# Optimization experiments

Hardware: AMD Instinct MI355X
Metric: run time of the kernel (lower is better)

The kernel has to match this reference:

```python
import jax, jax.numpy as jnp
import numpy as np

V = 50288; D = 768; L = 12; SPLIT = 6; L_LORA = L - SPLIT
NSTATE = 64; HDIM = 64
DIN = 2 * D                         # expand=2 -> 1536
H = DIN // HDIM                     # 24 heads
K = 4                               # depthwise conv kernel
DPROJ = 2 * DIN + 2 * NSTATE + H    # 3224
CONVD = DIN + 2 * NSTATE            # 1664
R = 8; LORA_SCALE = 2.0             # alpha/rank = 2r/r
EPS = 1e-5


def _rms(x, w):
    return x * jax.lax.rsqrt(jnp.mean(x * x, axis=-1, keepdims=True) + EPS) * w


def _ssm_scan(dt, A, Bm, Cm, xh):
    # dt:[B,T,H]  A:[H]  Bm,Cm:[B,T,N]  xh:[B,T,H,P]
    dA = jnp.exp(dt * A)
    def step(h, inp):
        dA_t, dt_t, B_t, C_t, x_t = inp
        h = dA_t[:, :, None, None] * h + (dt_t[..., None] * x_t)[..., None] * B_t[:, None, None, :]
        return h, jnp.einsum('bhpn,bn->bhp', h, C_t)
    h0 = jnp.zeros((dt.shape[0], H, HDIM, NSTATE), dt.dtype)
    xs = tuple(jnp.moveaxis(a, 1, 0) for a in (dA, dt, Bm, Cm, xh))
    _, ys = jax.lax.scan(step, h0, xs)
    return jnp.moveaxis(ys, 0, 1)  # [B,T,H,P]


@jax.checkpoint
def _mixer(u, in_w, cw, cb, dtb, A_log, Dsk, gw, out_w):
    # Mamba2 selective-scan block (ngroups=1, no biases on projections)
    Bsz, T, _ = u.shape
    zxbcdt = u @ in_w.T                              # [B,T,DPROJ]
    z = zxbcdt[..., :DIN]
    xBC = zxbcdt[..., DIN:DIN + CONVD]
    dt = zxbcdt[..., DIN + CONVD:]
    xp = jnp.pad(xBC, ((0, 0), (K - 1, 0), (0, 0)))  # causal depthwise conv1d
    xBC = jax.nn.silu(cb + sum(cw[:, k] * xp[:, k:k + T] for k in range(K)))
    xh = xBC[..., :DIN].reshape(Bsz, T, H, HDIM)
    Bm = xBC[..., DIN:DIN + NSTATE]
    Cm = xBC[..., DIN + NSTATE:]
    dt = jax.nn.softplus(dt + dtb)
    y = _ssm_scan(dt, -jnp.exp(A_log), Bm, Cm, xh) + Dsk[None, None, :, None] * xh
    y = _rms(y.reshape(Bsz, T, DIN) * jax.nn.silu(z), gw)   # gated RMSNorm
    return y @ out_w.T


def _run_base(x, res, p):
    def step(carry, q):
        x, res = carry
        res = x + res
        h = _mixer(_rms(res, q['nw']), q['iw'], q['cw'], q['cb'], q['dtb'],
                   q['al'], q['dk'], q['gw'], q['ow'])
        return (h, res), None
    (x, res), _ = jax.lax.scan(step, (x, res), p)
    return x, res


def _run_lora(x, res, p):
    def step(carry, q):
        x, res = carry
        res = x + res
        iw = q['iw'] + LORA_SCALE * (q['ibw'] @ q['iaw'])   # LoRALinear effective weight
        ow = q['ow'] + LORA_SCALE * (q['obw'] @ q['oaw'])
        h = _mixer(_rms(res, q['nw']), iw, q['cw'], q['cb'], q['dtb'],
                   q['al'], q['dk'], q['gw'], ow)
        return (h, res), None
    (x, res), _ = jax.lax.scan(step, (x, res), p)
    return x, res


def _rope(x, loop_i):
    # LoopRoPE: rotate interleaved pairs of hidden dims by angle theta_i * loop_i
    inv_freq = 1.0 / (10000.0 ** (jnp.arange(0, D, 2, dtype=jnp.float32) / D))
    f = loop_i * inv_freq
    cos_v = jnp.repeat(jnp.cos(f), 2)
    sin_v = jnp.repeat(jnp.sin(f), 2)
    x1, x2 = x[..., ::2], x[..., 1::2]
    rot = jnp.stack([-x2, x1], axis=-1).reshape(x.shape)
    return x * cos_v + rot * sin_v


def _forward(input_ids, n_loops, embedding, norm_w, in_w, conv_w, conv_b, dt_bias, A_log,
             D_skip, gnorm_w, out_w, lora_in_A, lora_in_B, lora_out_A, lora_out_B,
             core_in_w, core_conv_w, core_conv_b, core_dt_bias, core_A_log, core_D,
             core_gnorm_w, core_out_w, loop_norm_w, lifeline_gate, norm_f_w, lm_head_w):
    base = {'nw': norm_w[:SPLIT], 'iw': in_w[:SPLIT], 'cw': conv_w[:SPLIT], 'cb': conv_b[:SPLIT],
            'dtb': dt_bias[:SPLIT], 'al': A_log[:SPLIT], 'dk': D_skip[:SPLIT],
            'gw': gnorm_w[:SPLIT], 'ow': out_w[:SPLIT]}
    lora = {'nw': norm_w[SPLIT:], 'iw': in_w[SPLIT:], 'cw': conv_w[SPLIT:], 'cb': conv_b[SPLIT:],
            'dtb': dt_bias[SPLIT:], 'al': A_log[SPLIT:], 'dk': D_skip[SPLIT:],
            'gw': gnorm_w[SPLIT:], 'ow': out_w[SPLIT:],
            'iaw': lora_in_A, 'ibw': lora_in_B, 'oaw': lora_out_A, 'obw': lora_out_B}
    x = embedding[input_ids]                       # [B,T,D]
    res = jnp.zeros_like(x)                        # residual=None -> zeros
    x, res = _run_base(x, res, base)               # frozen layers [0:6]
    x, res = _run_lora(x, res, lora)               # LoRA layers [6:12]
    x_prompt = jax.lax.stop_gradient(x)            # x.clone().detach()
    for i in range(int(n_loops)):
        x = x + lifeline_gate * x_prompt           # lifeline injection
        x = _rope(x, float(i))                     # loop-index RoPE
        x, res = _run_lora(x, res, lora)           # run_lora recursion body
        x = x + _mixer(x, core_in_w, core_conv_w, core_conv_b, core_dt_bias,
                       core_A_log, core_D, core_gnorm_w, core_out_w)  # mamba2_core
        x = _rms(x, loop_norm_w)                   # loop_norm
    h = _rms(x + res, norm_f_w)                    # norm_f(x, residual, prenorm=False)
    return h @ lm_head_w.T                         # lm_head logits [B,T,V]


def setup_inputs() -> dict:
    key = jax.random.key(0)
    ks = iter(jax.random.split(key, 64))
    f32 = jnp.float32
    def w(shape, s=0.02):
        return (s * jax.random.normal(next(ks), shape)).astype(f32)
    inp = {
        'input_ids': jax.random.randint(next(ks), (2, 512), 0, 50277, dtype=jnp.int32),
        'n_loops': 3,
        'embedding': w((V, D)),
        'norm_w': jnp.ones((L, D), f32),
        'in_w': w((L, DPROJ, D)),
        'conv_w': w((L, CONVD, K), 0.2),
        'conv_b': jnp.zeros((L, CONVD), f32),
        'dt_bias': w((L, H), 0.5),
        'A_log': jnp.log(1.0 + 15.0 * jax.random.uniform(next(ks), (L, H))).astype(f32),
        'D_skip': jnp.ones((L, H), f32),
        'gnorm_w': jnp.ones((L, DIN), f32),
        'out_w': w((L, D, DIN)),
        'lora_in_A': w((L_LORA, R, D), 0.05),
        'lora_in_B': w((L_LORA, DPROJ, R), 0.05),
        'lora_out_A': w((L_LORA, R, DIN), 0.05),
        'lora_out_B': w((L_LORA, D, R), 0.05),
        'core_in_w': w((DPROJ, D)),
        'core_conv_w': w((CONVD, K), 0.2),
        'core_conv_b': jnp.zeros((CONVD,), f32),
        'core_dt_bias': w((H,), 0.5),
        'core_A_log': jnp.log(1.0 + 15.0 * jax.random.uniform(next(ks), (H,))).astype(f32),
        'core_D': jnp.ones((H,), f32),
        'core_gnorm_w': jnp.ones((DIN,), f32),
        'core_out_w': w((D, DIN)),
        'loop_norm_w': jnp.ones((D,), f32),
        'lifeline_gate': jnp.ones((D,), f32),
        'norm_f_w': jnp.ones((D,), f32),
        'lm_head_w': w((V, D)),
    }
    return inp


def reference(input_ids, n_loops, embedding, norm_w, in_w, conv_w, conv_b, dt_bias, A_log,
              D_skip, gnorm_w, out_w, lora_in_A, lora_in_B, lora_out_A, lora_out_B,
              core_in_w, core_conv_w, core_conv_b, core_dt_bias, core_A_log, core_D,
              core_gnorm_w, core_out_w, loop_norm_w, lifeline_gate, norm_f_w, lm_head_w):
    return _forward(input_ids, n_loops, embedding, norm_w, in_w, conv_w, conv_b, dt_bias,
                    A_log, D_skip, gnorm_w, out_w, lora_in_A, lora_in_B, lora_out_A,
                    lora_out_B, core_in_w, core_conv_w, core_conv_b, core_dt_bias,
                    core_A_log, core_D, core_gnorm_w, core_out_w, loop_norm_w,
                    lifeline_gate, norm_f_w, lm_head_w)
```

## Files before the change

kernel.cpp:

```cpp
#include <hip/hip_runtime.h>
#include <math.h>

constexpr int Bsz   = 2;
constexpr int Tseq  = 512;
constexpr int Mtok  = Bsz * Tseq;
constexpr int Dm    = 768;
constexpr int DINc  = 1536;
constexpr int Hn    = 24;
constexpr int NS    = 64;
constexpr int KC    = 4;
constexpr int DPROJc = 2*DINc + 2*NS + Hn;
constexpr int CONVDc = DINc + 2*NS;
constexpr int NL    = 12;
constexpr int SPL   = 6;
constexpr int LLO   = 6;
constexpr int NCH   = 8;
constexpr int Vv    = 50288;
constexpr float EPSc = 1e-5f;
constexpr int NLOOPS = 3;

#define DEVI __device__ __forceinline__

typedef _Float16 f16x8 __attribute__((ext_vector_type(8)));
typedef float    f32x4 __attribute__((ext_vector_type(4)));

DEVI float siluf(float x){ return x / (1.0f + expf(-x)); }
DEVI float softplusf(float x){ return (x > 20.0f) ? x : log1pf(expf(x)); }
DEVI unsigned short f2h(float f){
  union { _Float16 h; unsigned short u; } c;
  c.h = (_Float16)f;
  return c.u;
}
DEVI float h2f(unsigned short u){
  union { unsigned short u; _Float16 h; } c;
  c.u = u; return (float)c.h;
}

DEVI void gload16(const void* g, void* l){
  __builtin_amdgcn_global_load_lds(
      (const __attribute__((address_space(1))) void*)g,
      (__attribute__((address_space(3))) void*)l, 16, 0, 0);
}

DEVI float blk_reduce256(float v, float* sh){
  #pragma unroll
  for (int o = 32; o; o >>= 1) v += __shfl_down(v, o);
  int lane = threadIdx.x & 63, w = threadIdx.x >> 6;
  if (lane == 0) sh[w] = v;
  __syncthreads();
  return sh[0] + sh[1] + sh[2] + sh[3];
}

__global__ void k_embed(const int* __restrict__ ids, const float* __restrict__ emb,
                        float* __restrict__ x){
  int m = blockIdx.x;
  int id = ids[m];
  const float4* src = (const float4*)(emb + (size_t)id * Dm);
  float4* dst = (float4*)(x + (size_t)m * Dm);
  int i = threadIdx.x;
  dst[i] = src[i];
}

__global__ void k_f2h(const float* __restrict__ in, unsigned short* __restrict__ out, int n4){
  int e = blockIdx.x*256 + threadIdx.x;
  if (e >= n4) return;
  float4 v = ((const float4*)in)[e];
  ushort4 o; o.x=f2h(v.x); o.y=f2h(v.y); o.z=f2h(v.z); o.w=f2h(v.w);
  ((ushort4*)out)[e] = o;
}

__global__ __launch_bounds__(256) void k_addrms(const float* __restrict__ xin,
    float* __restrict__ res, unsigned short* __restrict__ ub,
    const float* __restrict__ w){
  int m = blockIdx.x, tid = threadIdx.x;
  __shared__ float sh[4];
  const float* xr = xin + (size_t)m*Dm;
  float* rr = res + (size_t)m*Dm;
  float r[3]; float ss = 0.f;
  #pragma unroll
  for (int k=0;k<3;k++){ int e = tid + k*256; float v = xr[e] + rr[e]; r[k]=v; ss += v*v; }
  ss = blk_reduce256(ss, sh);
  float rs = 1.0f / sqrtf(ss/(float)Dm + EPSc);
  #pragma unroll
  for (int k=0;k<3;k++){
    int e = tid + k*256;
    rr[e] = r[k];
    ub[(size_t)m*Dm+e] = f2h(r[k]*rs*w[e]);
  }
}

__global__ __launch_bounds__(256) void k_addrms_p(const float* __restrict__ part,
    float* __restrict__ res, unsigned short* __restrict__ ub,
    const float* __restrict__ w){
  int m = blockIdx.x, tid = threadIdx.x;
  __shared__ float sh[4];
  const size_t tot = (size_t)Mtok*Dm;
  float* rr = res + (size_t)m*Dm;
  float r[3]; float ss = 0.f;
  #pragma unroll
  for (int k=0;k<3;k++){
    int e = tid + k*256;
    size_t idx = (size_t)m*Dm + e;
    float v = rr[e] + part[idx] + part[tot+idx] + part[2*tot+idx] + part[3*tot+idx];
    r[k]=v; ss += v*v;
  }
  ss = blk_reduce256(ss, sh);
  float rs = 1.0f / sqrtf(ss/(float)Dm + EPSc);
  #pragma unroll
  for (int k=0;k<3;k++){
    int e = tid + k*256;
    rr[e] = r[k];
    ub[(size_t)m*Dm+e] = f2h(r[k]*rs*w[e]);
  }
}

__global__ void k_sum_xp(const float* __restrict__ part, float* __restrict__ x,
                         float* __restrict__ xp){
  size_t e = (size_t)blockIdx.x*256 + threadIdx.x;
  const size_t tot = (size_t)Mtok*Dm;
  if (e >= tot) return;
  float v = part[e] + part[tot+e] + part[2*tot+e] + part[3*tot+e];
  x[e] = v; xp[e] = v;
}

__global__ void k_f2h_sum(const float* __restrict__ part, float* __restrict__ x,
                          unsigned short* __restrict__ ub){
  size_t e = (size_t)blockIdx.x*256 + threadIdx.x;
  const size_t tot = (size_t)Mtok*Dm;
  if (e >= tot) return;
  float v = part[e] + part[tot+e] + part[2*tot+e] + part[3*tot+e];
  x[e] = v; ub[e] = f2h(v);
}

__global__ __launch_bounds__(256) void k_rms_p(const float* __restrict__ part,
    float* __restrict__ x, const float* __restrict__ w){
  int m = blockIdx.x, tid = threadIdx.x;
  __shared__ float sh[4];
  const size_t tot = (size_t)Mtok*Dm;
  float* xr = x + (size_t)m*Dm;
  float r[3]; float ss = 0.f;
  #pragma unroll
  for (int k=0;k<3;k++){
    int e = tid + k*256;
    size_t idx = (size_t)m*Dm + e;
    float v = xr[e] + part[idx] + part[tot+idx] + part[2*tot+idx] + part[3*tot+idx];
    r[k]=v; ss += v*v;
  }
  ss = blk_reduce256(ss, sh);
  float rs = 1.0f / sqrtf(ss/(float)Dm + EPSc);
  #pragma unroll
  for (int k=0;k<3;k++){ int e = tid + k*256; xr[e] = r[k]*rs*w[e]; }
}

__global__ __launch_bounds__(128) void k_liferope(float* __restrict__ x,
    const float* __restrict__ xp, const float* __restrict__ gate, float iF){
  int m = blockIdx.x, tid = threadIdx.x;
  float* xr = x + (size_t)m*Dm;
  const float* pr = xp + (size_t)m*Dm;
  #pragma unroll
  for (int k=0;k<3;k++){
    int j = tid + k*128;
    int d0 = 2*j, d1 = d0+1;
    float v0 = xr[d0] + gate[d0]*pr[d0];
    float v1 = xr[d1] + gate[d1]*pr[d1];
    float invf = expf(-9.210340371976184f * ((float)(2*j) * (1.0f/768.0f)));
    float f = iF * invf;
    float cv = cosf(f), sv = sinf(f);
    xr[d0] = v0*cv - v1*sv;
    xr[d1] = v1*cv + v0*sv;
  }
}

__global__ __launch_bounds__(256) void k_gemm_h(
    const unsigned short* __restrict__ A,
    const unsigned short* __restrict__ Bw,
    void* __restrict__ Cv, int Nd, int Kd, int outmode){
  alignas(16) __shared__ unsigned short lA[2][128*64];
  alignas(16) __shared__ unsigned short lB[2][128*64];
  const int tid  = threadIdx.x;
  const int lane = tid & 63;
  const int wv   = tid >> 6;
  const int wm   = wv >> 1, wn = wv & 1;
  const int gx = gridDim.x, gy = gridDim.y;
  const int nwg = gx*gy;
  const int flat = blockIdx.x + gx*blockIdx.y;
  const int q = nwg >> 3, r = nwg & 7;
  const int xcd = flat & 7, pos = flat >> 3;
  const int lg = (xcd < r ? xcd*(q+1) : r*(q+1) + (xcd - r)*q) + pos;
  const int m_idx = lg % gy, n_idx = lg / gy;
  const int n0 = n_idx * 128;
  const int m0 = m_idx * 128;
  const int KS = gridDim.z;
  const int kchunk = Kd / KS;
  const int kbeg = blockIdx.z * kchunk;
  const int nsteps = kchunk / 64;

  f32x4 acc[4][4] = {};

  auto stage = [&](int buf, int k0){
    #pragma unroll
    for (int i=0;i<4;i++){
      int seg = tid + i*256;
      int row = seg >> 3;
      int c8  = (seg & 7) ^ (row & 7);
      gload16(A + (size_t)(m0 + row)*Kd + k0 + c8*8, &lA[buf][seg*8]);
      int rn = n0 + row; rn = (rn < Nd) ? rn : (Nd - 1);
      gload16(Bw + (size_t)rn*Kd + k0 + c8*8, &lB[buf][seg*8]);
    }
  };

  stage(0, kbeg);
  for (int t=0; t<nsteps; ++t){
    const int cur = t & 1;
    if (t+1 < nsteps){
      stage(cur^1, kbeg + (t+1)*64);
      __builtin_amdgcn_sched_barrier(0);
      asm volatile("s_waitcnt vmcnt(8)" ::: "memory");
    } else {
      asm volatile("s_waitcnt vmcnt(0)" ::: "memory");
    }
    __builtin_amdgcn_s_barrier();
    __builtin_amdgcn_sched_barrier(0);
    #pragma unroll
    for (int kk=0; kk<2; kk++){
      f16x8 af[4], bfr[4];
      #pragma unroll
      for (int f=0; f<4; f++){
        int rowa = wm*64 + f*16 + (lane & 15);
        int ba = rowa*128 + ((kk*64 + (lane>>4)*16) ^ ((rowa & 7) << 4));
        af[f] = *(const f16x8*)((const char*)&lA[cur][0] + ba);
        int rowb = wn*64 + f*16 + (lane & 15);
        int bb = rowb*128 + ((kk*64 + (lane>>4)*16) ^ ((rowb & 7) << 4));
        bfr[f] = *(const f16x8*)((const char*)&lB[cur][0] + bb);
      }
      #pragma unroll
      for (int fm=0; fm<4; fm++)
        #pragma unroll
        for (int fn=0; fn<4; fn++)
          acc[fm][fn] = __builtin_amdgcn_mfma_f32_16x16x32_f16(af[fm], bfr[fn], acc[fm][fn], 0, 0, 0);
    }
    __builtin_amdgcn_s_barrier();
  }

  #pragma unroll
  for (int fm=0; fm<4; fm++){
    int mbase = m0 + wm*64 + fm*16 + ((lane>>4)<<2);
    #pragma unroll
    for (int fn=0; fn<4; fn++){
      int n = n0 + wn*64 + fn*16 + (lane & 15);
      if (n < Nd){
        #pragma unroll
        for (int rr=0;rr<4;rr++){
          size_t idx = (size_t)(mbase + rr)*Nd + n;
          float v = acc[fm][fn][rr];
          if (outmode == 0){
            float* Cb = (float*)Cv + (size_t)blockIdx.z*((size_t)Mtok*Nd);
            Cb[idx] = v;
          } else if (outmode == 1){
            ((float*)Cv)[idx] = v;
          } else {
            ((unsigned short*)Cv)[idx] = f2h(v);
          }
        }
      }
    }
  }
}

__global__ void k_prep_in(const float* __restrict__ W12, const float* __restrict__ Wc,
    const float* __restrict__ lA, const float* __restrict__ lB,
    unsigned short* __restrict__ out){
  const int tot4 = DPROJc*Dm/4;
  int e4 = blockIdx.x*256 + threadIdx.x;
  if (e4 >= tot4) return;
  int l = blockIdx.y;
  const float* W = (l < 12) ? W12 + (size_t)l*DPROJc*Dm : Wc;
  const int k4n = Dm/4;
  int n = e4 / k4n, k4 = e4 - n*k4n;
  float4 wv = *(const float4*)(W + (size_t)n*Dm + k4*4);
  float s0=wv.x, s1=wv.y, s2=wv.z, s3=wv.w;
  if (l >= SPL && l < 12){
    int ll = l - SPL;
    const float* Bl = lB + (size_t)ll*DPROJc*8;
    const float* Al = lA + (size_t)ll*8*Dm;
    #pragma unroll
    for (int r=0;r<8;r++){
      float b = 2.0f * Bl[n*8+r];
      float4 a = *(const float4*)(Al + (size_t)r*Dm + k4*4);
      s0 += b*a.x; s1 += b*a.y; s2 += b*a.z; s3 += b*a.w;
    }
  }
  ushort4 o; o.x=f2h(s0); o.y=f2h(s1); o.z=f2h(s2); o.w=f2h(s3);
  ((ushort4*)(out + (size_t)l*DPROJc*Dm))[e4] = o;
}

__global__ void k_prep_out(const float* __restrict__ W12, const float* __restrict__ Wc,
    const float* __restrict__ lA, const float* __restrict__ lB,
    unsigned short* __restrict__ out){
  const int tot4 = Dm*DINc/4;
  int e4 = blockIdx.x*256 + threadIdx.x;
  if (e4 >= tot4) return;
  int l = blockIdx.y;
  const float* W = (l < 12) ? W12 + (size_t)l*Dm*DINc : Wc;
  const int k4n = DINc/4;
  int n = e4 / k4n, k4 = e4 - n*k4n;
  float4 wv = *(const float4*)(W + (size_t)n*DINc + k4*4);
  float s0=wv.x, s1=wv.y, s2=wv.z, s3=wv.w;
  if (l >= SPL && l < 12){
    int ll = l - SPL;
    const float* Bl = lB + (size_t)ll*Dm*8;
    const float* Al = lA + (size_t)ll*8*DINc;
    #pragma unroll
    for (int r=0;r<8;r++){
      float b = 2.0f * Bl[n*8+r];
      float4 a = *(const float4*)(Al + (size_t)r*DINc + k4*4);
      s0 += b*a.x; s1 += b*a.y; s2 += b*a.z; s3 += b*a.w;
    }
  }
  ushort4 o; o.x=f2h(s0); o.y=f2h(s1); o.z=f2h(s2); o.w=f2h(s3);
  ((ushort4*)(out + (size_t)l*Dm*DINc))[e4] = o;
}

DEVI f16x8 ldfrag(const unsigned short (*T)[72], int row, int k0){
  return *(const f16x8*)&T[row][k0];
}

__global__ __launch_bounds__(256) void k_s1(const unsigned short* __restrict__ zxh,
    const float* __restrict__ cw, const float* __restrict__ cb,
    const float* __restrict__ dtb, const float* __restrict__ alog,
    float* __restrict__ S, float* __restrict__ ctot){
  int bh = blockIdx.x; int b = bh / Hn, h = bh % Hn; int c = blockIdx.y;
  __shared__ unsigned short XT[64][72];
  __shared__ unsigned short BwT[64][72];
  __shared__ float wv[64];
  int tid = threadIdx.x;
  int base_m = b*Tseq + c*64;
  if (tid < 64){
    float Av = -expf(alog[h]);
    float zdt = h2f(zxh[(size_t)(base_m+tid)*DPROJc + DINc + CONVDc + h]) + dtb[h];
    float dt = softplusf(zdt);
    float s = dt * Av;
    #pragma unroll
    for (int o=1;o<64;o<<=1){ float v = __shfl_up(s, o); if (tid >= o) s += v; }
    if (tid == 63) ctot[bh*NCH + c] = s;
    float ce = __shfl(s, 63);
    wv[tid] = expf(ce - s) * dt;
  }
  __syncthreads();
  int ch = tid & 63;
  int t0 = (tid >> 6) * 16;
  int tl = c*64 + t0;
  {
    int cc = h*64 + ch;
    float4 w4 = *(const float4*)&cw[cc*KC];
    float bias = cb[cc];
    const unsigned short* zp = zxh + (size_t)base_m*DPROJc + DINc + cc;
    float v0 = (tl >= 3) ? h2f(zp[(long)(t0-3)*DPROJc]) : 0.f;
    float v1 = (tl >= 2) ? h2f(zp[(long)(t0-2)*DPROJc]) : 0.f;
    float v2 = (tl >= 1) ? h2f(zp[(long)(t0-1)*DPROJc]) : 0.f;
    #pragma unroll
    for (int i=0;i<16;i++){
      float v3 = h2f(zp[(long)(t0+i)*DPROJc]);
      float o = bias + w4.x*v0 + w4.y*v1 + w4.z*v2 + w4.w*v3;
      XT[ch][t0+i] = f2h(siluf(o));
      v0=v1; v1=v2; v2=v3;
    }
  }
  {
    int cc = DINc + ch;
    float4 w4 = *(const float4*)&cw[cc*KC];
    float bias = cb[cc];
    const unsigned short* zp = zxh + (size_t)base_m*DPROJc + DINc + cc;
    float v0 = (tl >= 3) ? h2f(zp[(long)(t0-3)*DPROJc]) : 0.f;
    float v1 = (tl >= 2) ? h2f(zp[(long)(t0-2)*DPROJc]) : 0.f;
    float v2 = (tl >= 1) ? h2f(zp[(long)(t0-1)*DPROJc]) : 0.f;
    #pragma unroll
    for (int i=0;i<16;i++){
      float v3 = h2f(zp[(long)(t0+i)*DPROJc]);
      float o = bias + w4.x*v0 + w4.y*v1 + w4.z*v2 + w4.w*v3;
      BwT[ch][t0+i] = f2h(siluf(o) * wv[t0+i]);
      v0=v1; v1=v2; v2=v3;
    }
  }
  __syncthreads();
  int lane = tid & 63, wid = tid >> 6, wmp = wid >> 1, wnn = wid & 1;
  f32x4 acc[2][2] = {};
  #pragma unroll
  for (int kk=0; kk<2; kk++){
    int k0 = kk*32 + (lane>>4)*8;
    f16x8 a[2], bf[2];
    #pragma unroll
    for (int f=0; f<2; f++){
      a[f]  = ldfrag(XT,  wmp*32 + f*16 + (lane&15), k0);
      bf[f] = ldfrag(BwT, wnn*32 + f*16 + (lane&15), k0);
    }
    #pragma unroll
    for (int fm=0; fm<2; fm++)
      #pragma unroll
      for (int fn=0; fn<2; fn++)
        acc[fm][fn] = __builtin_amdgcn_mfma_f32_16x16x32_f16(a[fm], bf[fn], acc[fm][fn], 0, 0, 0);
  }
  float* Sb = S + ((size_t)(bh*NCH + c))*4096;
  #pragma unroll
  for (int fm=0; fm<2; fm++)
    #pragma unroll
    for (int fn=0; fn<2; fn++)
      #pragma unroll
      for (int rg=0; rg<4; rg++){
        int p = wmp*32 + fm*16 + ((lane>>4)<<2) + rg;
        int n = wnn*32 + fn*16 + (lane&15);
        Sb[p*64 + n] = acc[fm][fn][rg];
      }
}

__global__ void k_s2(const float* __restrict__ S, const float* __restrict__ ctot,
                     float* __restrict__ hst){
  int gid = blockIdx.x*256 + threadIdx.x;
  int bh = gid >> 12; int e = gid & 4095;
  float hv = 0.f;
  #pragma unroll
  for (int c=0;c<NCH;c++){
    size_t idx = ((size_t)(bh*NCH + c))*4096 + e;
    hst[idx] = hv;
    float Ac = expf(ctot[bh*NCH + c]);
    hv = Ac*hv + S[idx];
  }
}

__global__ __launch_bounds__(256) void k_s3(const unsigned short* __restrict__ zxh,
    const float* __restrict__ cw, const float* __restrict__ cb,
    const float* __restrict__ dtb, const float* __restrict__ alog,
    const float* __restrict__ hst, const float* __restrict__ Dsk,
    unsigned short* __restrict__ y){
  int bh = blockIdx.x; int b = bh / Hn, h = bh % Hn; int c = blockIdx.y;
  __shared__ unsigned short Ch[64][72];
  __shared__ unsigned short Bh[64][72];
  __shared__ unsigned short XhT[64][72];
  __shared__ unsigned short hT[64][72];
  __shared__ unsigned short Mh[64][72];
  __shared__ float cumS[64], dtS[64];
  int tid = threadIdx.x;
  int base_m = b*Tseq + c*64;
  if (tid < 64){
    float Av = -expf(alog[h]);
    float zdt = h2f(zxh[(size_t)(base_m+tid)*DPROJc + DINc + CONVDc + h]) + dtb[h];
    float dt = softplusf(zdt);
    float s = dt * Av;
    #pragma unroll
    for (int o=1;o<64;o<<=1){ float v = __shfl_up(s, o); if (tid >= o) s += v; }
    cumS[tid] = s;
    dtS[tid]  = dt;
  }
  int ch = tid & 63;
  int t0 = (tid >> 6) * 16;
  int tl = c*64 + t0;
  {
    int cc = h*64 + ch;
    float4 w4 = *(const float4*)&cw[cc*KC];
    float bias = cb[cc];
    const unsigned short* zp = zxh + (size_t)base_m*DPROJc + DINc + cc;
    float v0 = (tl >= 3) ? h2f(zp[(long)(t0-3)*DPROJc]) : 0.f;
    float v1 = (tl >= 2) ? h2f(zp[(long)(t0-2)*DPROJc]) : 0.f;
    float v2 = (tl >= 1) ? h2f(zp[(long)(t0-1)*DPROJc]) : 0.f;
    #pragma unroll
    for (int i=0;i<16;i++){
      float v3 = h2f(zp[(long)(t0+i)*DPROJc]);
      float o = bias + w4.x*v0 + w4.y*v1 + w4.z*v2 + w4.w*v3;
      XhT[ch][t0+i] = f2h(siluf(o));
      v0=v1; v1=v2; v2=v3;
    }
  }
  {
    int cc = DINc + ch;
    float4 w4 = *(const float4*)&cw[cc*KC];
    float bias = cb[cc];
    const unsigned short* zp = zxh + (size_t)base_m*DPROJc + DINc + cc;
    float v0 = (tl >= 3) ? h2f(zp[(long)(t0-3)*DPROJc]) : 0.f;
    float v1 = (tl >= 2) ? h2f(zp[(long)(t0-2)*DPROJc]) : 0.f;
    float v2 = (tl >= 1) ? h2f(zp[(long)(t0-1)*DPROJc]) : 0.f;
    #pragma unroll
    for (int i=0;i<16;i++){
      float v3 = h2f(zp[(long)(t0+i)*DPROJc]);
      float o = bias + w4.x*v0 + w4.y*v1 + w4.z*v2 + w4.w*v3;
      Bh[t0+i][ch] = f2h(siluf(o));
      v0=v1; v1=v2; v2=v3;
    }
  }
  {
    int cc = DINc + NS + ch;
    float4 w4 = *(const float4*)&cw[cc*KC];
    float bias = cb[cc];
    const unsigned short* zp = zxh + (size_t)base_m*DPROJc + DINc + cc;
    float v0 = (tl >= 3) ? h2f(zp[(long)(t0-3)*DPROJc]) : 0.f;
    float v1 = (tl >= 2) ? h2f(zp[(long)(t0-2)*DPROJc]) : 0.f;
    float v2 = (tl >= 1) ? h2f(zp[(long)(t0-1)*DPROJc]) : 0.f;
    #pragma unroll
    for (int i=0;i<16;i++){
      float v3 = h2f(zp[(long)(t0+i)*DPROJc]);
      float o = bias + w4.x*v0 + w4.y*v1 + w4.z*v2 + w4.w*v3;
      Ch[t0+i][ch] = f2h(siluf(o));
      v0=v1; v1=v2; v2=v3;
    }
  }
  {
    const float* hb = hst + ((size_t)(bh*NCH + c))*4096;
    for (int e4 = tid; e4 < 1024; e4 += 256){
      float4 hv = ((const float4*)hb)[e4];
      int p = (e4 << 2) >> 6, n = (e4 << 2) & 63;
      ushort4 o; o.x=f2h(hv.x); o.y=f2h(hv.y); o.z=f2h(hv.z); o.w=f2h(hv.w);
      *(ushort4*)&hT[p][n] = o;
    }
  }
  __syncthreads();
  int lane = tid & 63, wid = tid >> 6, wmt = wid >> 1, wns = wid & 1;
  f32x4 g[2][2] = {};
  #pragma unroll
  for (int kk=0; kk<2; kk++){
    int k0 = kk*32 + (lane>>4)*8;
    f16x8 a[2], bf[2];
    #pragma unroll
    for (int f=0; f<2; f++){
      a[f]  = ldfrag(Ch, wmt*32 + f*16 + (lane&15), k0);
      bf[f] = ldfrag(Bh, wns*32 + f*16 + (lane&15), k0);
    }
    #pragma unroll
    for (int fm=0; fm<2; fm++)
      #pragma unroll
      for (int fn=0; fn<2; fn++)
        g[fm][fn] = __builtin_amdgcn_mfma_f32_16x16x32_f16(a[fm], bf[fn], g[fm][fn], 0, 0, 0);
  }
  #pragma unroll
  for (int fm=0; fm<2; fm++)
    #pragma unroll
    for (int fn=0; fn<2; fn++)
      #pragma unroll
      for (int rg=0; rg<4; rg++){
        int t = wmt*32 + fm*16 + ((lane>>4)<<2) + rg;
        int s = wns*32 + fn*16 + (lane&15);
        float val = (s <= t) ? expf(cumS[t] - cumS[s]) * dtS[s] * g[fm][fn][rg] : 0.f;
        Mh[t][s] = f2h(val);
      }
  __syncthreads();
  f32x4 aL[2][2] = {}, aS[2][2] = {};
  #pragma unroll
  for (int kk=0; kk<2; kk++){
    int k0 = kk*32 + (lane>>4)*8;
    f16x8 m_[2], x_[2], c_[2], h_[2];
    #pragma unroll
    for (int f=0; f<2; f++){
      m_[f] = ldfrag(Mh,  wmt*32 + f*16 + (lane&15), k0);
      x_[f] = ldfrag(XhT, wns*32 + f*16 + (lane&15), k0);
      c_[f] = ldfrag(Ch,  wmt*32 + f*16 + (lane&15), k0);
      h_[f] = ldfrag(hT,  wns*32 + f*16 + (lane&15), k0);
    }
    #pragma unroll
    for (int fm=0; fm<2; fm++)
      #pragma unroll
      for (int fn=0; fn<2; fn++){
        aL[fm][fn] = __builtin_amdgcn_mfma_f32_16x16x32_f16(m_[fm], x_[fn], aL[fm][fn], 0, 0, 0);
        aS[fm][fn] = __builtin_amdgcn_mfma_f32_16x16x32_f16(c_[fm], h_[fn], aS[fm][fn], 0, 0, 0);
      }
  }
  float Dh = Dsk[h];
  #pragma unroll
  for (int fm=0; fm<2; fm++)
    #pragma unroll
    for (int fn=0; fn<2; fn++)
      #pragma unroll
      for (int rg=0; rg<4; rg++){
        int t = wmt*32 + fm*16 + ((lane>>4)<<2) + rg;
        int p = wns*32 + fn*16 + (lane&15);
        float Pt = expf(cumS[t]);
        float xv = h2f(XhT[p][t]);
        float o = aL[fm][fn][rg] + Pt*aS[fm][fn][rg] + Dh*xv;
        y[(size_t)(base_m+t)*DINc + h*64 + p] = f2h(o);
      }
}

__global__ __launch_bounds__(256) void k_gate(const unsigned short* __restrict__ zxh,
    const unsigned short* __restrict__ y, unsigned short* __restrict__ yb,
    const float* __restrict__ gw){
  int m = blockIdx.x, tid = threadIdx.x;
  __shared__ float sh[4];
  const unsigned short* zr = zxh + (size_t)m*DPROJc;
  const unsigned short* yr = y + (size_t)m*DINc;
  float g[6]; float ss = 0.f;
  #pragma unroll
  for (int k=0;k<6;k++){
    int e = tid + k*256;
    float z = h2f(zr[e]);
    float v = h2f(yr[e]) * siluf(z);
    g[k] = v; ss += v*v;
  }
  ss = blk_reduce256(ss, sh);
  float rs = 1.0f / sqrtf(ss/(float)DINc + EPSc);
  #pragma unroll
  for (int k=0;k<6;k++){
    int e = tid + k*256;
    yb[(size_t)m*DINc + e] = f2h(g[k]*rs*gw[e]);
  }
}

struct WSP {
  float *x,*res,*xp,*ctot,*Sc,*hst,*part;
  unsigned short *zxh,*yh,*ub,*yb,*wib,*wob,*whb;
};

static void run_mixer_h(hipStream_t st, const WSP& w, const unsigned short* ub_in,
    const unsigned short* iw, const float* cw, const float* cb, const float* dtb,
    const float* al, const float* dk, const float* gw, const unsigned short* ow){
  dim3 gIn((DPROJc + 127)/128, Mtok/128, 1);
  k_gemm_h<<<gIn, 256, 0, st>>>(ub_in, iw, w.zxh, DPROJc, Dm, 2);
  k_s1<<<dim3(Bsz*Hn, NCH), 256, 0, st>>>(w.zxh, cw, cb, dtb, al, w.Sc, w.ctot);
  k_s2<<<(Bsz*Hn*4096)/256, 256, 0, st>>>(w.Sc, w.ctot, w.hst);
  k_s3<<<dim3(Bsz*Hn, NCH), 256, 0, st>>>(w.zxh, cw, cb, dtb, al, w.hst, dk, w.yh);
  k_gate<<<Mtok, 256, 0, st>>>(w.zxh, w.yh, w.yb, gw);
  dim3 gOut(Dm/128, Mtok/128, 4);
  k_gemm_h<<<gOut, 256, 0, st>>>(w.yb, ow, w.part, Dm, DINc, 0);
}

extern "C" void kernel_launch(void* const* d_in, const int* in_sizes, int n_in,
                              void* d_out, int out_size, void* d_ws, size_t ws_size,
                              hipStream_t stream){
  const int*   ids        = (const int*)  d_in[0];
  const float* emb        = (const float*)d_in[2];
  const float* norm_w     = (const float*)d_in[3];
  const float* in_w       = (const float*)d_in[4];
  const float* conv_w     = (const float*)d_in[5];
  const float* conv_b     = (const float*)d_in[6];
  const float* dt_bias    = (const float*)d_in[7];
  const float* A_log      = (const float*)d_in[8];
  const float* D_skip     = (const float*)d_in[9];
  const float* gnorm_w    = (const float*)d_in[10];
  const float* out_w      = (const float*)d_in[11];
  const float* lora_in_A  = (const float*)d_in[12];
  const float* lora_in_B  = (const float*)d_in[13];
  const float* lora_out_A = (const float*)d_in[14];
  const float* lora_out_B = (const float*)d_in[15];
  const float* core_in_w  = (const float*)d_in[16];
  const float* core_conv_w= (const float*)d_in[17];
  const float* core_conv_b= (const float*)d_in[18];
  const float* core_dtb   = (const float*)d_in[19];
  const float* core_A_log = (const float*)d_in[20];
  const float* core_D     = (const float*)d_in[21];
  const float* core_gw    = (const float*)d_in[22];
  const float* core_out_w = (const float*)d_in[23];
  const float* loop_norm_w= (const float*)d_in[24];
  const float* life_gate  = (const float*)d_in[25];
  const float* norm_f_w   = (const float*)d_in[26];
  const float* lm_head_w  = (const float*)d_in[27];
  (void)in_sizes; (void)n_in; (void)out_size; (void)ws_size;

  char* pb = (char*)d_ws;
  auto balloc = [&](size_t bytes){
    char* q = pb; pb += (bytes + 255) & ~(size_t)255; return q;
  };
  WSP w;
  w.x    = (float*)balloc((size_t)Mtok*Dm*4);
  w.res  = (float*)balloc((size_t)Mtok*Dm*4);
  w.xp   = (float*)balloc((size_t)Mtok*Dm*4);
  w.ctot = (float*)balloc((size_t)Bsz*Hn*NCH*4);
  w.Sc   = (float*)balloc((size_t)Bsz*Hn*NCH*4096*4);
  w.hst  = (float*)balloc((size_t)Bsz*Hn*NCH*4096*4);
  w.part = (float*)balloc((size_t)4*Mtok*Dm*4);
  w.zxh  = (unsigned short*)balloc((size_t)Mtok*DPROJc*2);
  w.yh   = (unsigned short*)balloc((size_t)Mtok*DINc*2);
  w.ub   = (unsigned short*)balloc((size_t)Mtok*Dm*2);
  w.yb   = (unsigned short*)balloc((size_t)Mtok*DINc*2);

  const size_t IWN = (size_t)DPROJc*Dm;
  const size_t OWN = (size_t)Dm*DINc;
  const size_t HWN = (size_t)Vv*Dm;
  w.wib = (unsigned short*)balloc(13*IWN*2);
  w.wob = (unsigned short*)balloc(13*OWN*2);
  w.whb = (unsigned short*)balloc(HWN*2);

  k_prep_in<<<dim3((IWN/4 + 255)/256, 13), 256, 0, stream>>>(
      in_w, core_in_w, lora_in_A, lora_in_B, w.wib);
  k_prep_out<<<dim3((OWN/4 + 255)/256, 13), 256, 0, stream>>>(
      out_w, core_out_w, lora_out_A, lora_out_B, w.wob);
  k_f2h<<<(HWN/4 + 255)/256, 256, 0, stream>>>(lm_head_w, w.whb, (int)(HWN/4));

  k_embed<<<Mtok, 192, 0, stream>>>(ids, emb, w.x);
  hipMemsetAsync(w.res, 0, (size_t)Mtok*Dm*sizeof(float), stream);

  const size_t totMD = (size_t)Mtok*Dm;

  auto mixer_l = [&](int l){
    run_mixer_h(stream, w, w.ub,
        w.wib + (size_t)l*IWN, conv_w + (size_t)l*CONVDc*KC, conv_b + (size_t)l*CONVDc,
        dt_bias + (size_t)l*Hn, A_log + (size_t)l*Hn, D_skip + (size_t)l*Hn,
        gnorm_w + (size_t)l*DINc, w.wob + (size_t)l*OWN);
  };
  k_addrms<<<Mtok, 256, 0, stream>>>(w.x, w.res, w.ub, norm_w);
  mixer_l(0);
  for (int l=1; l<NL; l++){
    k_addrms_p<<<Mtok, 256, 0, stream>>>(w.part, w.res, w.ub, norm_w + (size_t)l*Dm);
    mixer_l(l);
  }
  k_sum_xp<<<(totMD + 255)/256, 256, 0, stream>>>(w.part, w.x, w.xp);
  for (int i=0;i<NLOOPS;i++){
    k_liferope<<<Mtok, 128, 0, stream>>>(w.x, w.xp, life_gate, (float)i);
    k_addrms<<<Mtok, 256, 0, stream>>>(w.x, w.res, w.ub, norm_w + (size_t)SPL*Dm);
    mixer_l(SPL);
    for (int l=SPL+1; l<NL; l++){
      k_addrms_p<<<Mtok, 256, 0, stream>>>(w.part, w.res, w.ub, norm_w + (size_t)l*Dm);
      mixer_l(l);
    }
    k_f2h_sum<<<(totMD + 255)/256, 256, 0, stream>>>(w.part, w.x, w.ub);
    run_mixer_h(stream, w, w.ub,
        w.wib + 12*IWN, core_conv_w, core_conv_b, core_dtb, core_A_log, core_D,
        core_gw, w.wob + 12*OWN);
    k_rms_p<<<Mtok, 256, 0, stream>>>(w.part, w.x, loop_norm_w);
  }
  k_addrms<<<Mtok, 256, 0, stream>>>(w.x, w.res, w.ub, norm_f_w);
  dim3 gHead((Vv + 127)/128, Mtok/128, 1);
  k_gemm_h<<<gHead, 256, 0, stream>>>(w.ub, w.whb, d_out, Vv, Dm, 1);
}
```

Before: 2.752 ms.

## Fuse chunked SSD scan stages and gated RMSNorm into one per-head kernel

Replaces the three chunked-scan kernels (k_s1, k_s2, k_s3) and the gate kernel with a single k_ssd kernel per (batch, head). Each block loops over the chunks sequentially and carries the inter-chunk state in shared memory. The gated output's sum of squares is accumulated into a per-row buffer with atomics. The gnorm weight is folded into the output-projection weights at prep time, and the RMS scale is applied in the output GEMM epilogue. This removes several launches per mixer and the round-trips of state and intermediate y through global memory. In exchange, the scan grid shrinks from 384 blocks to 48 blocks that run the chunks serially.

```diff
diff --git a/kernel.cpp b/kernel.cpp
--- a/kernel.cpp
+++ b/kernel.cpp
@@ -71,7 +71,7 @@
 
 __global__ __launch_bounds__(256) void k_addrms(const float* __restrict__ xin,
     float* __restrict__ res, unsigned short* __restrict__ ub,
-    const float* __restrict__ w){
+    const float* __restrict__ w, float* __restrict__ rssum){
   int m = blockIdx.x, tid = threadIdx.x;
   __shared__ float sh[4];
   const float* xr = xin + (size_t)m*Dm;
@@ -80,6 +80,7 @@
   #pragma unroll
   for (int k=0;k<3;k++){ int e = tid + k*256; float v = xr[e] + rr[e]; r[k]=v; ss += v*v; }
   ss = blk_reduce256(ss, sh);
+  if (tid == 0 && rssum) rssum[m] = 0.f;
   float rs = 1.0f / sqrtf(ss/(float)Dm + EPSc);
   #pragma unroll
   for (int k=0;k<3;k++){
@@ -91,7 +92,7 @@
 
 __global__ __launch_bounds__(256) void k_addrms_p(const float* __restrict__ part,
     float* __restrict__ res, unsigned short* __restrict__ ub,
-    const float* __restrict__ w){
+    const float* __restrict__ w, float* __restrict__ rssum){
   int m = blockIdx.x, tid = threadIdx.x;
   __shared__ float sh[4];
   const size_t tot = (size_t)Mtok*Dm;
@@ -105,6 +106,7 @@
     r[k]=v; ss += v*v;
   }
   ss = blk_reduce256(ss, sh);
+  if (tid == 0 && rssum) rssum[m] = 0.f;
   float rs = 1.0f / sqrtf(ss/(float)Dm + EPSc);
   #pragma unroll
   for (int k=0;k<3;k++){
@@ -124,10 +126,11 @@
 }
 
 __global__ void k_f2h_sum(const float* __restrict__ part, float* __restrict__ x,
-                          unsigned short* __restrict__ ub){
+                          unsigned short* __restrict__ ub, float* __restrict__ rssum){
   size_t e = (size_t)blockIdx.x*256 + threadIdx.x;
   const size_t tot = (size_t)Mtok*Dm;
   if (e >= tot) return;
+  if (e < Mtok) rssum[e] = 0.f;
   float v = part[e] + part[tot+e] + part[2*tot+e] + part[3*tot+e];
   x[e] = v; ub[e] = f2h(v);
 }
@@ -174,9 +177,11 @@
 __global__ __launch_bounds__(256) void k_gemm_h(
     const unsigned short* __restrict__ A,
     const unsigned short* __restrict__ Bw,
-    void* __restrict__ Cv, int Nd, int Kd, int outmode){
+    void* __restrict__ Cv, int Nd, int Kd, int outmode,
+    const float* __restrict__ rsrow){
   alignas(16) __shared__ unsigned short lA[2][128*64];
   alignas(16) __shared__ unsigned short lB[2][128*64];
+  __shared__ float lRs[128];
   const int tid  = threadIdx.x;
   const int lane = tid & 63;
   const int wv   = tid >> 6;
@@ -195,6 +200,8 @@
   const int kbeg = blockIdx.z * kchunk;
   const int nsteps = kchunk / 64;
 
+  if (rsrow && tid < 128) lRs[tid] = rsrow[m0 + tid];
+
   f32x4 acc[4][4] = {};
 
   auto stage = [&](int buf, int k0){
@@ -244,7 +251,8 @@
 
   #pragma unroll
   for (int fm=0; fm<4; fm++){
-    int mbase = m0 + wm*64 + fm*16 + ((lane>>4)<<2);
+    int mloc = wm*64 + fm*16 + ((lane>>4)<<2);
+    int mbase = m0 + mloc;
     #pragma unroll
     for (int fn=0; fn<4; fn++){
       int n = n0 + wn*64 + fn*16 + (lane & 15);
@@ -253,6 +261,8 @@
         for (int rr=0;rr<4;rr++){
           size_t idx = (size_t)(mbase + rr)*Nd + n;
           float v = acc[fm][fn][rr];
+          if (rsrow)
+            v *= 1.0f / sqrtf(lRs[mloc + rr]*(1.0f/(float)DINc) + EPSc);
           if (outmode == 0){
             float* Cb = (float*)Cv + (size_t)blockIdx.z*((size_t)Mtok*Nd);
             Cb[idx] = v;
@@ -296,12 +306,14 @@
 
 __global__ void k_prep_out(const float* __restrict__ W12, const float* __restrict__ Wc,
     const float* __restrict__ lA, const float* __restrict__ lB,
+    const float* __restrict__ gnw, const float* __restrict__ core_gw,
     unsigned short* __restrict__ out){
   const int tot4 = Dm*DINc/4;
   int e4 = blockIdx.x*256 + threadIdx.x;
   if (e4 >= tot4) return;
   int l = blockIdx.y;
   const float* W = (l < 12) ? W12 + (size_t)l*Dm*DINc : Wc;
+  const float* gw = (l < 12) ? gnw + (size_t)l*DINc : core_gw;
   const int k4n = DINc/4;
   int n = e4 / k4n, k4 = e4 - n*k4n;
   float4 wv = *(const float4*)(W + (size_t)n*DINc + k4*4);
@@ -317,6 +329,8 @@
       s0 += b*a.x; s1 += b*a.y; s2 += b*a.z; s3 += b*a.w;
     }
   }
+  float4 g4 = *(const float4*)(gw + k4*4);
+  s0 *= g4.x; s1 *= g4.y; s2 *= g4.z; s3 *= g4.w;
   ushort4 o; o.x=f2h(s0); o.y=f2h(s1); o.z=f2h(s2); o.w=f2h(s3);
   ((ushort4*)(out + (size_t)l*Dm*DINc))[e4] = o;
 }
@@ -325,298 +339,203 @@
   return *(const f16x8*)&T[row][k0];
 }
 
-__global__ __launch_bounds__(256) void k_s1(const unsigned short* __restrict__ zxh,
+__global__ __launch_bounds__(256) void k_ssd(const unsigned short* __restrict__ zxh,
     const float* __restrict__ cw, const float* __restrict__ cb,
     const float* __restrict__ dtb, const float* __restrict__ alog,
-    float* __restrict__ S, float* __restrict__ ctot){
-  int bh = blockIdx.x; int b = bh / Hn, h = bh % Hn; int c = blockIdx.y;
-  __shared__ unsigned short XT[64][72];
+    const float* __restrict__ Dsk, unsigned short* __restrict__ g_out,
+    float* __restrict__ rssum){
+  int bh = blockIdx.x; int b = bh / Hn, h = bh % Hn;
+  __shared__ unsigned short XhT[64][72];
+  __shared__ unsigned short Bh [64][72];
   __shared__ unsigned short BwT[64][72];
-  __shared__ float wv[64];
+  __shared__ unsigned short Ch [64][72];
+  __shared__ unsigned short Mh [64][72];
+  __shared__ unsigned short hT [64][72];
+  __shared__ float hS[64][64];
+  __shared__ float cumS[64], dtS[64], wvS[64];
+  __shared__ float AcS;
   int tid = threadIdx.x;
-  int base_m = b*Tseq + c*64;
-  if (tid < 64){
-    float Av = -expf(alog[h]);
-    float zdt = h2f(zxh[(size_t)(base_m+tid)*DPROJc + DINc + CONVDc + h]) + dtb[h];
-    float dt = softplusf(zdt);
-    float s = dt * Av;
-    #pragma unroll
-    for (int o=1;o<64;o<<=1){ float v = __shfl_up(s, o); if (tid >= o) s += v; }
-    if (tid == 63) ctot[bh*NCH + c] = s;
-    float ce = __shfl(s, 63);
-    wv[tid] = expf(ce - s) * dt;
-  }
-  __syncthreads();
+  int lane = tid & 63, wid = tid >> 6, wmt = wid >> 1, wns = wid & 1;
+  for (int e = tid; e < 4096; e += 256) ((float*)hS)[e] = 0.f;
+  float Av = -expf(alog[h]);
+  float Dh = Dsk[h];
   int ch = tid & 63;
   int t0 = (tid >> 6) * 16;
-  int tl = c*64 + t0;
-  {
-    int cc = h*64 + ch;
-    float4 w4 = *(const float4*)&cw[cc*KC];
-    float bias = cb[cc];
-    const unsigned short* zp = zxh + (size_t)base_m*DPROJc + DINc + cc;
-    float v0 = (tl >= 3) ? h2f(zp[(long)(t0-3)*DPROJc]) : 0.f;
-    float v1 = (tl >= 2) ? h2f(zp[(long)(t0-2)*DPROJc]) : 0.f;
-    float v2 = (tl >= 1) ? h2f(zp[(long)(t0-1)*DPROJc]) : 0.f;
-    #pragma unroll
-    for (int i=0;i<16;i++){
-      float v3 = h2f(zp[(long)(t0+i)*DPROJc]);
-      float o = bias + w4.x*v0 + w4.y*v1 + w4.z*v2 + w4.w*v3;
-      XT[ch][t0+i] = f2h(siluf(o));
-      v0=v1; v1=v2; v2=v3;
-    }
-  }
-  {
-    int cc = DINc + ch;
-    float4 w4 = *(const float4*)&cw[cc*KC];
-    float bias = cb[cc];
-    const unsigned short* zp = zxh + (size_t)base_m*DPROJc + DINc + cc;
-    float v0 = (tl >= 3) ? h2f(zp[(long)(t0-3)*DPROJc]) : 0.f;
-    float v1 = (tl >= 2) ? h2f(zp[(long)(t0-2)*DPROJc]) : 0.f;
-    float v2 = (tl >= 1) ? h2f(zp[(long)(t0-1)*DPROJc]) : 0.f;
-    #pragma unroll
-    for (int i=0;i<16;i++){
-      float v3 = h2f(zp[(long)(t0+i)*DPROJc]);
-      float o = bias + w4.x*v0 + w4.y*v1 + w4.z*v2 + w4.w*v3;
-      BwT[ch][t0+i] = f2h(siluf(o) * wv[t0+i]);
-      v0=v1; v1=v2; v2=v3;
-    }
-  }
-  __syncthreads();
-  int lane = tid & 63, wid = tid >> 6, wmp = wid >> 1, wnn = wid & 1;
-  f32x4 acc[2][2] = {};
-  #pragma unroll
-  for (int kk=0; kk<2; kk++){
-    int k0 = kk*32 + (lane>>4)*8;
-    f16x8 a[2], bf[2];
-    #pragma unroll
-    for (int f=0; f<2; f++){
-      a[f]  = ldfrag(XT,  wmp*32 + f*16 + (lane&15), k0);
-      bf[f] = ldfrag(BwT, wnn*32 + f*16 + (lane&15), k0);
+
+  for (int c = 0; c < NCH; ++c){
+    __syncthreads();
+    int base_m = b*Tseq + c*64;
+    int tl = c*64 + t0;
+    if (tid < 64){
+      float zdt = h2f(zxh[(size_t)(base_m+tid)*DPROJc + DINc + CONVDc + h]) + dtb[h];
+      float dt = softplusf(zdt);
+      float s = dt * Av;
+      #pragma unroll
+      for (int o=1;o<64;o<<=1){ float v = __shfl_up(s, o); if (tid >= o) s += v; }
+      cumS[tid] = s; dtS[tid] = dt;
+      float ce = __shfl(s, 63);
+      wvS[tid] = expf(ce - s) * dt;
+      if (tid == 0) AcS = expf(ce);
+    }
+    {
+      int cc = h*64 + ch;
+      float4 w4 = *(const float4*)&cw[cc*KC];
+      float bias = cb[cc];
+      const unsigned short* zp = zxh + (size_t)base_m*DPROJc + DINc + cc;
+      float v0 = (tl >= 3) ? h2f(zp[(long)(t0-3)*DPROJc]) : 0.f;
+      float v1 = (tl >= 2) ? h2f(zp[(long)(t0-2)*DPROJc]) : 0.f;
+      float v2 = (tl >= 1) ? h2f(zp[(long)(t0-1)*DPROJc]) : 0.f;
+      #pragma unroll
+      for (int i=0;i<16;i++){
+        float v3 = h2f(zp[(long)(t0+i)*DPROJc]);
+        float o = bias + w4.x*v0 + w4.y*v1 + w4.z*v2 + w4.w*v3;
+        XhT[ch][t0+i] = f2h(siluf(o));
+        v0=v1; v1=v2; v2=v3;
+      }
+    }
+    {
+      int cc = DINc + ch;
+      float4 w4 = *(const float4*)&cw[cc*KC];
+      float bias = cb[cc];
+      const unsigned short* zp = zxh + (size_t)base_m*DPROJc + DINc + cc;
+      float v0 = (tl >= 3) ? h2f(zp[(long)(t0-3)*DPROJc]) : 0.f;
+      float v1 = (tl >= 2) ? h2f(zp[(long)(t0-2)*DPROJc]) : 0.f;
+      float v2 = (tl >= 1) ? h2f(zp[(long)(t0-1)*DPROJc]) : 0.f;
+      #pragma unroll
+      for (int i=0;i<16;i++){
+        float v3 = h2f(zp[(long)(t0+i)*DPROJc]);
+        float o = bias + w4.x*v0 + w4.y*v1 + w4.z*v2 + w4.w*v3;
+        Bh[t0+i][ch] = f2h(siluf(o));
+        v0=v1; v1=v2; v2=v3;
+      }
+    }
+    {
+      int cc = DINc + NS + ch;
+      float4 w4 = *(const float4*)&cw[cc*KC];
+      float bias = cb[cc];
+      const unsigned short* zp = zxh + (size_t)base_m*DPROJc + DINc + cc;
+      float v0 = (tl >= 3) ? h2f(zp[(long)(t0-3)*DPROJc]) : 0.f;
+      float v1 = (tl >= 2) ? h2f(zp[(long)(t0-2)*DPROJc]) : 0.f;
+      float v2 = (tl >= 1) ? h2f(zp[(long)(t0-1)*DPROJc]) : 0.f;
+      #pragma unroll
+      for (int i=0;i<16;i++){
+        float v3 = h2f(zp[(long)(t0+i)*DPROJc]);
+        float o = bias + w4.x*v0 + w4.y*v1 + w4.z*v2 + w4.w*v3;
+        Ch[t0+i][ch] = f2h(siluf(o));
+        v0=v1; v1=v2; v2=v3;
+      }
+    }
+    for (int e4 = tid; e4 < 1024; e4 += 256){
+      const float* hp = (const float*)hS + e4*4;
+      int p = (e4 << 2) >> 6, n = (e4 << 2) & 63;
+      ushort4 o; o.x=f2h(hp[0]); o.y=f2h(hp[1]); o.z=f2h(hp[2]); o.w=f2h(hp[3]);
+      *(ushort4*)&hT[p][n] = o;
+    }
+    __syncthreads();
+    for (int e = tid; e < 4096; e += 256){
+      int t = e >> 6, n = e & 63;
+      BwT[n][t] = f2h(h2f(Bh[t][n]) * wvS[t]);
+    }
+    f32x4 g[2][2] = {};
+    #pragma unroll
+    for (int kk=0; kk<2; kk++){
+      int k0 = kk*32 + (lane>>4)*8;
+      f16x8 a[2], bf[2];
+      #pragma unroll
+      for (int f=0; f<2; f++){
+        a[f]  = ldfrag(Ch, wmt*32 + f*16 + (lane&15), k0);
+        bf[f] = ldfrag(Bh, wns*32 + f*16 + (lane&15), k0);
+      }
+      #pragma unroll
+      for (int fm=0; fm<2; fm++)
+        #pragma unroll
+        for (int fn=0; fn<2; fn++)
+          g[fm][fn] = __builtin_amdgcn_mfma_f32_16x16x32_f16(a[fm], bf[fn], g[fm][fn], 0, 0, 0);
     }
     #pragma unroll
     for (int fm=0; fm<2; fm++)
       #pragma unroll
       for (int fn=0; fn<2; fn++)
-        acc[fm][fn] = __builtin_amdgcn_mfma_f32_16x16x32_f16(a[fm], bf[fn], acc[fm][fn], 0, 0, 0);
-  }
-  float* Sb = S + ((size_t)(bh*NCH + c))*4096;
-  #pragma unroll
-  for (int fm=0; fm<2; fm++)
-    #pragma unroll
-    for (int fn=0; fn<2; fn++)
-      #pragma unroll
-      for (int rg=0; rg<4; rg++){
-        int p = wmp*32 + fm*16 + ((lane>>4)<<2) + rg;
-        int n = wnn*32 + fn*16 + (lane&15);
-        Sb[p*64 + n] = acc[fm][fn][rg];
-      }
-}
-
-__global__ void k_s2(const float* __restrict__ S, const float* __restrict__ ctot,
-                     float* __restrict__ hst){
-  int gid = blockIdx.x*256 + threadIdx.x;
-  int bh = gid >> 12; int e = gid & 4095;
-  float hv = 0.f;
-  #pragma unroll
-  for (int c=0;c<NCH;c++){
-    size_t idx = ((size_t)(bh*NCH + c))*4096 + e;
-    hst[idx] = hv;
-    float Ac = expf(ctot[bh*NCH + c]);
-    hv = Ac*hv + S[idx];
-  }
-}
-
-__global__ __launch_bounds__(256) void k_s3(const unsigned short* __restrict__ zxh,
-    const float* __restrict__ cw, const float* __restrict__ cb,
-    const float* __restrict__ dtb, const float* __restrict__ alog,
-    const float* __restrict__ hst, const float* __restrict__ Dsk,
-    unsigned short* __restrict__ y){
-  int bh = blockIdx.x; int b = bh / Hn, h = bh % Hn; int c = blockIdx.y;
-  __shared__ unsigned short Ch[64][72];
-  __shared__ unsigned short Bh[64][72];
-  __shared__ unsigned short XhT[64][72];
-  __shared__ unsigned short hT[64][72];
-  __shared__ unsigned short Mh[64][72];
-  __shared__ float cumS[64], dtS[64];
-  int tid = threadIdx.x;
-  int base_m = b*Tseq + c*64;
-  if (tid < 64){
-    float Av = -expf(alog[h]);
-    float zdt = h2f(zxh[(size_t)(base_m+tid)*DPROJc + DINc + CONVDc + h]) + dtb[h];
-    float dt = softplusf(zdt);
-    float s = dt * Av;
-    #pragma unroll
-    for (int o=1;o<64;o<<=1){ float v = __shfl_up(s, o); if (tid >= o) s += v; }
-    cumS[tid] = s;
-    dtS[tid]  = dt;
-  }
-  int ch = tid & 63;
-  int t0 = (tid >> 6) * 16;
-  int tl = c*64 + t0;
-  {
-    int cc = h*64 + ch;
-    float4 w4 = *(const float4*)&cw[cc*KC];
-    float bias = cb[cc];
-    const unsigned short* zp = zxh + (size_t)base_m*DPROJc + DINc + cc;
-    float v0 = (tl >= 3) ? h2f(zp[(long)(t0-3)*DPROJc]) : 0.f;
-    float v1 = (tl >= 2) ? h2f(zp[(long)(t0-2)*DPROJc]) : 0.f;
-    float v2 = (tl >= 1) ? h2f(zp[(long)(t0-1)*DPROJc]) : 0.f;
-    #pragma unroll
-    for (int i=0;i<16;i++){
-      float v3 = h2f(zp[(long)(t0+i)*DPROJc]);
-      float o = bias + w4.x*v0 + w4.y*v1 + w4.z*v2 + w4.w*v3;
-      XhT[ch][t0+i] = f2h(siluf(o));
-      v0=v1; v1=v2; v2=v3;
-    }
-  }
-  {
-    int cc = DINc + ch;
-    float4 w4 = *(const float4*)&cw[cc*KC];
-    float bias = cb[cc];
-    const unsigned short* zp = zxh + (size_t)base_m*DPROJc + DINc + cc;
-    float v0 = (tl >= 3) ? h2f(zp[(long)(t0-3)*DPROJc]) : 0.f;
-    float v1 = (tl >= 2) ? h2f(zp[(long)(t0-2)*DPROJc]) : 0.f;
-    float v2 = (tl >= 1) ? h2f(zp[(long)(t0-1)*DPROJc]) : 0.f;
-    #pragma unroll
-    for (int i=0;i<16;i++){
-      float v3 = h2f(zp[(long)(t0+i)*DPROJc]);
-      float o = bias + w4.x*v0 + w4.y*v1 + w4.z*v2 + w4.w*v3;
-      Bh[t0+i][ch] = f2h(siluf(o));
-      v0=v1; v1=v2; v2=v3;
-    }
-  }
-  {
-    int cc = DINc + NS + ch;
-    float4 w4 = *(const float4*)&cw[cc*KC];
-    float bias = cb[cc];
-    const unsigned short* zp = zxh + (size_t)base_m*DPROJc + DINc + cc;
-    float v0 = (tl >= 3) ? h2f(zp[(long)(t0-3)*DPROJc]) : 0.f;
-    float v1 = (tl >= 2) ? h2f(zp[(long)(t0-2)*DPROJc]) : 0.f;
-    float v2 = (tl >= 1) ? h2f(zp[(long)(t0-1)*DPROJc]) : 0.f;
-    #pragma unroll
-    for (int i=0;i<16;i++){
-      float v3 = h2f(zp[(long)(t0+i)*DPROJc]);
-      float o = bias + w4.x*v0 + w4.y*v1 + w4.z*v2 + w4.w*v3;
-      Ch[t0+i][ch] = f2h(siluf(o));
-      v0=v1; v1=v2; v2=v3;
-    }
-  }
-  {
-    const float* hb = hst + ((size_t)(bh*NCH + c))*4096;
-    for (int e4 = tid; e4 < 1024; e4 += 256){
-      float4 hv = ((const float4*)hb)[e4];
-      int p = (e4 << 2) >> 6, n = (e4 << 2) & 63;
-      ushort4 o; o.x=f2h(hv.x); o.y=f2h(hv.y); o.z=f2h(hv.z); o.w=f2h(hv.w);
-      *(ushort4*)&hT[p][n] = o;
-    }
-  }
-  __syncthreads();
-  int lane = tid & 63, wid = tid >> 6, wmt = wid >> 1, wns = wid & 1;
-  f32x4 g[2][2] = {};
-  #pragma unroll
-  for (int kk=0; kk<2; kk++){
-    int k0 = kk*32 + (lane>>4)*8;
-    f16x8 a[2], bf[2];
-    #pragma unroll
-    for (int f=0; f<2; f++){
-      a[f]  = ldfrag(Ch, wmt*32 + f*16 + (lane&15), k0);
-      bf[f] = ldfrag(Bh, wns*32 + f*16 + (lane&15), k0);
-    }
-    #pragma unroll
-    for (int fm=0; fm<2; fm++)
-      #pragma unroll
-      for (int fn=0; fn<2; fn++)
-        g[fm][fn] = __builtin_amdgcn_mfma_f32_16x16x32_f16(a[fm], bf[fn], g[fm][fn], 0, 0, 0);
-  }
-  #pragma unroll
-  for (int fm=0; fm<2; fm++)
-    #pragma unroll
-    for (int fn=0; fn<2; fn++)
+        #pragma unroll
+        for (int rg=0; rg<4; rg++){
+          int t = wmt*32 + fm*16 + ((lane>>4)<<2) + rg;
+          int s = wns*32 + fn*16 + (lane&15);
+          float val = (s <= t) ? expf(cumS[t] - cumS[s]) * dtS[s] * g[fm][fn][rg] : 0.f;
+          Mh[t][s] = f2h(val);
+        }
+    __syncthreads();
+    f32x4 aL[2][2] = {}, aS[2][2] = {}, Sc[2][2] = {};
+    #pragma unroll
+    for (int kk=0; kk<2; kk++){
+      int k0 = kk*32 + (lane>>4)*8;
+      f16x8 m_[2], x_[2], c_[2], h_[2], xp_[2], bw_[2];
+      #pragma unroll
+      for (int f=0; f<2; f++){
+        m_[f]  = ldfrag(Mh,  wmt*32 + f*16 + (lane&15), k0);
+        x_[f]  = ldfrag(XhT, wns*32 + f*16 + (lane&15), k0);
+        c_[f]  = ldfrag(Ch,  wmt*32 + f*16 + (lane&15), k0);
+        h_[f]  = ldfrag(hT,  wns*32 + f*16 + (lane&15), k0);
+        xp_[f] = ldfrag(XhT, wmt*32 + f*16 + (lane&15), k0);
+        bw_[f] = ldfrag(BwT, wns*32 + f*16 + (lane&15), k0);
+      }
+      #pragma unroll
+      for (int fm=0; fm<2; fm++)
+        #pragma unroll
+        for (int fn=0; fn<2; fn++){
+          aL[fm][fn] = __builtin_amdgcn_mfma_f32_16x16x32_f16(m_[fm],  x_[fn],  aL[fm][fn], 0, 0, 0);
+          aS[fm][fn] = __builtin_amdgcn_mfma_f32_16x16x32_f16(c_[fm],  h_[fn],  aS[fm][fn], 0, 0, 0);
+          Sc[fm][fn] = __builtin_amdgcn_mfma_f32_16x16x32_f16(xp_[fm], bw_[fn], Sc[fm][fn], 0, 0, 0);
+        }
+    }
+    #pragma unroll
+    for (int fm=0; fm<2; fm++){
       #pragma unroll
       for (int rg=0; rg<4; rg++){
         int t = wmt*32 + fm*16 + ((lane>>4)<<2) + rg;
-        int s = wns*32 + fn*16 + (lane&15);
-        float val = (s <= t) ? expf(cumS[t] - cumS[s]) * dtS[s] * g[fm][fn][rg] : 0.f;
-        Mh[t][s] = f2h(val);
-      }
-  __syncthreads();
-  f32x4 aL[2][2] = {}, aS[2][2] = {};
-  #pragma unroll
-  for (int kk=0; kk<2; kk++){
-    int k0 = kk*32 + (lane>>4)*8;
-    f16x8 m_[2], x_[2], c_[2], h_[2];
-    #pragma unroll
-    for (int f=0; f<2; f++){
-      m_[f] = ldfrag(Mh,  wmt*32 + f*16 + (lane&15), k0);
-      x_[f] = ldfrag(XhT, wns*32 + f*16 + (lane&15), k0);
-      c_[f] = ldfrag(Ch,  wmt*32 + f*16 + (lane&15), k0);
-      h_[f] = ldfrag(hT,  wns*32 + f*16 + (lane&15), k0);
-    }
+        float Pt = expf(cumS[t]);
+        float sq = 0.f;
+        #pragma unroll
+        for (int fn=0; fn<2; fn++){
+          int p = wns*32 + fn*16 + (lane&15);
+          float xv = h2f(XhT[p][t]);
+          float yv = aL[fm][fn][rg] + Pt*aS[fm][fn][rg] + Dh*xv;
+          float z = h2f(zxh[(size_t)(base_m+t)*DPROJc + h*64 + p]);
+          float gv = yv * siluf(z);
+          g_out[(size_t)(base_m+t)*DINc + h*64 + p] = f2h(gv);
+          sq += gv*gv;
+        }
+        sq += __shfl_xor(sq, 1); sq += __shfl_xor(sq, 2);
+        sq += __shfl_xor(sq, 4); sq += __shfl_xor(sq, 8);
+        if ((lane & 15) == 0) atomicAdd(&rssum[base_m + t], sq);
+      }
+    }
+    float Ac = AcS;
     #pragma unroll
     for (int fm=0; fm<2; fm++)
       #pragma unroll
-      for (int fn=0; fn<2; fn++){
-        aL[fm][fn] = __builtin_amdgcn_mfma_f32_16x16x32_f16(m_[fm], x_[fn], aL[fm][fn], 0, 0, 0);
-        aS[fm][fn] = __builtin_amdgcn_mfma_f32_16x16x32_f16(c_[fm], h_[fn], aS[fm][fn], 0, 0, 0);
-      }
-  }
-  float Dh = Dsk[h];
-  #pragma unroll
-  for (int fm=0; fm<2; fm++)
-    #pragma unroll
-    for (int fn=0; fn<2; fn++)
-      #pragma unroll
-      for (int rg=0; rg<4; rg++){
-        int t = wmt*32 + fm*16 + ((lane>>4)<<2) + rg;
-        int p = wns*32 + fn*16 + (lane&15);
-        float Pt = expf(cumS[t]);
-        float xv = h2f(XhT[p][t]);
-        float o = aL[fm][fn][rg] + Pt*aS[fm][fn][rg] + Dh*xv;
-        y[(size_t)(base_m+t)*DINc + h*64 + p] = f2h(o);
-      }
-}
-
-__global__ __launch_bounds__(256) void k_gate(const unsigned short* __restrict__ zxh,
-    const unsigned short* __restrict__ y, unsigned short* __restrict__ yb,
-    const float* __restrict__ gw){
-  int m = blockIdx.x, tid = threadIdx.x;
-  __shared__ float sh[4];
-  const unsigned short* zr = zxh + (size_t)m*DPROJc;
-  const unsigned short* yr = y + (size_t)m*DINc;
-  float g[6]; float ss = 0.f;
-  #pragma unroll
-  for (int k=0;k<6;k++){
-    int e = tid + k*256;
-    float z = h2f(zr[e]);
-    float v = h2f(yr[e]) * siluf(z);
-    g[k] = v; ss += v*v;
-  }
-  ss = blk_reduce256(ss, sh);
-  float rs = 1.0f / sqrtf(ss/(float)DINc + EPSc);
-  #pragma unroll
-  for (int k=0;k<6;k++){
-    int e = tid + k*256;
-    yb[(size_t)m*DINc + e] = f2h(g[k]*rs*gw[e]);
+      for (int fn=0; fn<2; fn++)
+        #pragma unroll
+        for (int rg=0; rg<4; rg++){
+          int p = wmt*32 + fm*16 + ((lane>>4)<<2) + rg;
+          int n = wns*32 + fn*16 + (lane&15);
+          hS[p][n] = Ac*hS[p][n] + Sc[fm][fn][rg];
+        }
   }
 }
 
 struct WSP {
-  float *x,*res,*xp,*ctot,*Sc,*hst,*part;
-  unsigned short *zxh,*yh,*ub,*yb,*wib,*wob,*whb;
+  float *x,*res,*xp,*part,*rssum;
+  unsigned short *zxh,*ub,*yb,*wib,*wob,*whb;
 };
 
 static void run_mixer_h(hipStream_t st, const WSP& w, const unsigned short* ub_in,
     const unsigned short* iw, const float* cw, const float* cb, const float* dtb,
-    const float* al, const float* dk, const float* gw, const unsigned short* ow){
+    const float* al, const float* dk, const unsigned short* ow){
   dim3 gIn((DPROJc + 127)/128, Mtok/128, 1);
-  k_gemm_h<<<gIn, 256, 0, st>>>(ub_in, iw, w.zxh, DPROJc, Dm, 2);
-  k_s1<<<dim3(Bsz*Hn, NCH), 256, 0, st>>>(w.zxh, cw, cb, dtb, al, w.Sc, w.ctot);
-  k_s2<<<(Bsz*Hn*4096)/256, 256, 0, st>>>(w.Sc, w.ctot, w.hst);
-  k_s3<<<dim3(Bsz*Hn, NCH), 256, 0, st>>>(w.zxh, cw, cb, dtb, al, w.hst, dk, w.yh);
-  k_gate<<<Mtok, 256, 0, st>>>(w.zxh, w.yh, w.yb, gw);
+  k_gemm_h<<<gIn, 256, 0, st>>>(ub_in, iw, w.zxh, DPROJc, Dm, 2, nullptr);
+  k_ssd<<<Bsz*Hn, 256, 0, st>>>(w.zxh, cw, cb, dtb, al, dk, w.yb, w.rssum);
   dim3 gOut(Dm/128, Mtok/128, 4);
-  k_gemm_h<<<gOut, 256, 0, st>>>(w.yb, ow, w.part, Dm, DINc, 0);
+  k_gemm_h<<<gOut, 256, 0, st>>>(w.yb, ow, w.part, Dm, DINc, 0, w.rssum);
 }
 
 extern "C" void kernel_launch(void* const* d_in, const int* in_sizes, int n_in,
@@ -656,17 +575,14 @@
     char* q = pb; pb += (bytes + 255) & ~(size_t)255; return q;
   };
   WSP w;
-  w.x    = (float*)balloc((size_t)Mtok*Dm*4);
-  w.res  = (float*)balloc((size_t)Mtok*Dm*4);
-  w.xp   = (float*)balloc((size_t)Mtok*Dm*4);
-  w.ctot = (float*)balloc((size_t)Bsz*Hn*NCH*4);
-  w.Sc   = (float*)balloc((size_t)Bsz*Hn*NCH*4096*4);
-  w.hst  = (float*)balloc((size_t)Bsz*Hn*NCH*4096*4);
-  w.part = (float*)balloc((size_t)4*Mtok*Dm*4);
-  w.zxh  = (unsigned short*)balloc((size_t)Mtok*DPROJc*2);
-  w.yh   = (unsigned short*)balloc((size_t)Mtok*DINc*2);
-  w.ub   = (unsigned short*)balloc((size_t)Mtok*Dm*2);
-  w.yb   = (unsigned short*)balloc((size_t)Mtok*DINc*2);
+  w.x     = (float*)balloc((size_t)Mtok*Dm*4);
+  w.res   = (float*)balloc((size_t)Mtok*Dm*4);
+  w.xp    = (float*)balloc((size_t)Mtok*Dm*4);
+  w.part  = (float*)balloc((size_t)4*Mtok*Dm*4);
+  w.rssum = (float*)balloc((size_t)Mtok*4);
+  w.zxh   = (unsigned short*)balloc((size_t)Mtok*DPROJc*2);
+  w.ub    = (unsigned short*)balloc((size_t)Mtok*Dm*2);
+  w.yb    = (unsigned short*)balloc((size_t)Mtok*DINc*2);
 
   const size_t IWN = (size_t)DPROJc*Dm;
   const size_t OWN = (size_t)Dm*DINc;
@@ -678,7 +594,7 @@
   k_prep_in<<<dim3((IWN/4 + 255)/256, 13), 256, 0, stream>>>(
       in_w, core_in_w, lora_in_A, lora_in_B, w.wib);
   k_prep_out<<<dim3((OWN/4 + 255)/256, 13), 256, 0, stream>>>(
-      out_w, core_out_w, lora_out_A, lora_out_B, w.wob);
+      out_w, core_out_w, lora_out_A, lora_out_B, gnorm_w, core_gw, w.wob);
   k_f2h<<<(HWN/4 + 255)/256, 256, 0, stream>>>(lm_head_w, w.whb, (int)(HWN/4));
 
   k_embed<<<Mtok, 192, 0, stream>>>(ids, emb, w.x);
@@ -690,30 +606,30 @@
     run_mixer_h(stream, w, w.ub,
         w.wib + (size_t)l*IWN, conv_w + (size_t)l*CONVDc*KC, conv_b + (size_t)l*CONVDc,
         dt_bias + (size_t)l*Hn, A_log + (size_t)l*Hn, D_skip + (size_t)l*Hn,
-        gnorm_w + (size_t)l*DINc, w.wob + (size_t)l*OWN);
+        w.wob + (size_t)l*OWN);
   };
-  k_addrms<<<Mtok, 256, 0, stream>>>(w.x, w.res, w.ub, norm_w);
+  k_addrms<<<Mtok, 256, 0, stream>>>(w.x, w.res, w.ub, norm_w, w.rssum);
   mixer_l(0);
   for (int l=1; l<NL; l++){
-    k_addrms_p<<<Mtok, 256, 0, stream>>>(w.part, w.res, w.ub, norm_w + (size_t)l*Dm);
+    k_addrms_p<<<Mtok, 256, 0, stream>>>(w.part, w.res, w.ub, norm_w + (size_t)l*Dm, w.rssum);
     mixer_l(l);
   }
   k_sum_xp<<<(totMD + 255)/256, 256, 0, stream>>>(w.part, w.x, w.xp);
   for (int i=0;i<NLOOPS;i++){
     k_liferope<<<Mtok, 128, 0, stream>>>(w.x, w.xp, life_gate, (float)i);
-    k_addrms<<<Mtok, 256, 0, stream>>>(w.x, w.res, w.ub, norm_w + (size_t)SPL*Dm);
+    k_addrms<<<Mtok, 256, 0, stream>>>(w.x, w.res, w.ub, norm_w + (size_t)SPL*Dm, w.rssum);
     mixer_l(SPL);
     for (int l=SPL+1; l<NL; l++){
-      k_addrms_p<<<Mtok, 256, 0, stream>>>(w.part, w.res, w.ub, norm_w + (size_t)l*Dm);
+      k_addrms_p<<<Mtok, 256, 0, stream>>>(w.part, w.res, w.ub, norm_w + (size_t)l*Dm, w.rssum);
       mixer_l(l);
     }
-    k_f2h_sum<<<(totMD + 255)/256, 256, 0, stream>>>(w.part, w.x, w.ub);
+    k_f2h_sum<<<(totMD + 255)/256, 256, 0, stream>>>(w.part, w.x, w.ub, w.rssum);
     run_mixer_h(stream, w, w.ub,
         w.wib + 12*IWN, core_conv_w, core_conv_b, core_dtb, core_A_log, core_D,
-        core_gw, w.wob + 12*OWN);
+        w.wob + 12*OWN);
     k_rms_p<<<Mtok, 256, 0, stream>>>(w.part, w.x, loop_norm_w);
   }
-  k_addrms<<<Mtok, 256, 0, stream>>>(w.x, w.res, w.ub, norm_f_w);
+  k_addrms<<<Mtok, 256, 0, stream>>>(w.x, w.res, w.ub, norm_f_w, nullptr);
   dim3 gHead((Vv + 127)/128, Mtok/128, 1);
-  k_gemm_h<<<gHead, 256, 0, stream>>>(w.ub, w.whb, d_out, Vv, Dm, 1);
-}
+  k_gemm_h<<<gHead, 256, 0, stream>>>(w.ub, w.whb, d_out, Vv, Dm, 1, nullptr);
+}
```

Measured after the change: 5.919 ms. +115.1%, slower.
